# Kernel optimization log

Measured on AMD Instinct MI355X. Metric: run time of the kernel, lower is better.

## Reference

```python
import jax, jax.numpy as jnp
import numpy as np

NEG_INF = -4294967295.0  # -2**32 + 1, matches original padding value

def prelu(x, alpha):
    return jnp.where(x >= 0, x, alpha * x)

def setup_inputs() -> dict:
    key = jax.random.key(0)
    ks = jax.random.split(key, 12)
    B, T, D = 2048, 200, 64
    H0, H1 = 80, 40
    q = jax.random.normal(ks[0], (B, D), dtype=jnp.float32)
    k = jax.random.normal(ks[1], (B, T, D), dtype=jnp.float32)
    v = jax.random.normal(ks[2], (B, T, D), dtype=jnp.float32)
    mask = jax.random.randint(ks[3], (B, T), 0, 2, dtype=jnp.int32)
    Fin = 4 * D  # concat of q, k, q-k, q*k
    W0 = jax.random.normal(ks[4], (Fin, H0), dtype=jnp.float32) / np.sqrt(Fin)
    b0 = jnp.zeros((H0,), dtype=jnp.float32)
    a0 = jax.random.uniform(ks[5], (H0,), dtype=jnp.float32) * 0.25  # PReLU per-feature alpha
    W1 = jax.random.normal(ks[6], (H0, H1), dtype=jnp.float32) / np.sqrt(H0)
    b1 = jnp.zeros((H1,), dtype=jnp.float32)
    a1 = jax.random.uniform(ks[7], (H1,), dtype=jnp.float32) * 0.25
    Wo = jax.random.normal(ks[8], (H1, 1), dtype=jnp.float32) / np.sqrt(H1)
    bo = jnp.zeros((1,), dtype=jnp.float32)
    return {"q": q, "k": k, "v": v, "W0": W0, "b0": b0, "a0": a0,
            "W1": W1, "b1": b1, "a1": a1, "Wo": Wo, "bo": bo, "mask": mask}

def reference(q, k, v, W0, b0, a0, W1, b1, a1, Wo, bo, mask):
    # q: [B,D] -> broadcast to [B,T,D] (tile+reshape in original)
    qe = jnp.broadcast_to(q[:, None, :], k.shape)
    info = jnp.concatenate([qe, k, qe - k, qe * k], axis=-1)  # [B,T,4D]
    h = prelu(jnp.einsum('btf,fh->bth', info, W0) + b0, a0)    # [B,T,H0]
    h = prelu(jnp.einsum('bth,hg->btg', h, W1) + b1, a1)       # [B,T,H1]
    logits = (jnp.einsum('btg,go->bto', h, Wo) + bo)[..., 0]   # [B,T]
    logits = jnp.where(mask == 0, NEG_INF, logits)
    w = jax.nn.softmax(logits, axis=-1)                        # [B,T]
    out = jnp.einsum('bt,btd->bd', w, v)                       # [B,D]
    return out
```

## Files before the change

### kernel.cpp

```cpp
#include <hip/hip_runtime.h>
#include <math.h>

constexpr int D  = 64;
constexpr int T  = 200;
constexpr int H0 = 80;
constexpr int H1 = 40;
constexpr int BLOCK = 256;
constexpr float NEG_INF_V = -4294967295.0f;

typedef short short8 __attribute__((ext_vector_type(8)));
typedef float f32x4 __attribute__((ext_vector_type(4)));

__device__ inline void split_bf16(float x, unsigned short& hi, unsigned short& lo) {
    union { float f; unsigned u; } a; a.f = x;
    unsigned r = a.u + 0x7FFF + ((a.u >> 16) & 1);
    hi = (unsigned short)(r >> 16);
    union { unsigned u; float f; } h; h.u = (unsigned)hi << 16;
    union { float f; unsigned u; } bvu; bvu.f = x - h.f;
    unsigned r2 = bvu.u + 0x7FFF + ((bvu.u >> 16) & 1);
    lo = (unsigned short)(r2 >> 16);
}

__global__ __launch_bounds__(BLOCK, 2) void attn_fused(
    const float* __restrict__ q, const float* __restrict__ k,
    const float* __restrict__ v, const float* __restrict__ W0,
    const float* __restrict__ b0, const float* __restrict__ a0,
    const float* __restrict__ W1, const float* __restrict__ b1,
    const float* __restrict__ a1, const float* __restrict__ Wo,
    const int* __restrict__ mask, float* __restrict__ out)
{
    __shared__ unsigned short s_wfHi[5120];
    __shared__ unsigned short s_wfLo[5120];
    __shared__ unsigned short s_w1Hi[4608];
    __shared__ unsigned short s_w1Lo[4608];
    __shared__ unsigned short s_h0hi[4][16 * 80];
    __shared__ unsigned short s_h0lo[4][16 * 80];
    __shared__ float s_logits[208];
    __shared__ float s_biasq[H0];
    __shared__ float s_a0[H0];
    __shared__ float s_b1p[48], s_a1p[48], s_Wop[48];
    __shared__ float s_w[BLOCK];
    __shared__ float s_red[8];
    __shared__ float s_part[4][D];

    const int tid  = threadIdx.x;
    const int b    = blockIdx.x;
    const int wv   = tid >> 6;
    const int lane = tid & 63;
    const int l16  = lane & 15;
    const int quad = lane >> 4;
    const float* qb = q + (size_t)b * D;

    const int mval = (tid < T) ? mask[(size_t)b * T + tid] : 0;
    float4 kc[4];
    {
        int row = wv * 16 + l16; if (row > T - 1) row = T - 1;
        const float* kr = k + ((size_t)b * T + row) * D + quad * 8;
        kc[0] = *(const float4*)(kr);
        kc[1] = *(const float4*)(kr + 4);
        kc[2] = *(const float4*)(kr + 32);
        kc[3] = *(const float4*)(kr + 36);
    }

    const float* Wk = W0 + 64 * H0;
    const float* Wd = W0 + 128 * H0;
    const float* Wp = W0 + 192 * H0;
    #pragma unroll 4
    for (int it = 0; it < 20; ++it) {
        const int e  = it * 256 + tid;
        const int kk = e / 80, n = e - kk * 80;
        const float w = Wk[e] - Wd[e] + qb[kk] * Wp[e];
        unsigned short h, l; split_bf16(w, h, l);
        const int off = (((kk >> 5) * 5 + (n >> 4)) << 9)
                      + ((((kk >> 3) & 3) * 16 + (n & 15)) << 3) + (kk & 7);
        s_wfHi[off] = h; s_wfLo[off] = l;
    }
    #pragma unroll 4
    for (int it = 0; it < 18; ++it) {
        const int e  = it * 256 + tid;
        const int k2 = e / 48, n = e - k2 * 48;
        const float w = (k2 < H0 && n < H1) ? W1[k2 * H1 + n] : 0.0f;
        unsigned short h, l; split_bf16(w, h, l);
        const int off = (((k2 >> 5) * 3 + (n >> 4)) << 9)
                      + ((((k2 >> 3) & 3) * 16 + (n & 15)) << 3) + (k2 & 7);
        s_w1Hi[off] = h; s_w1Lo[off] = l;
    }
    if (tid < H0) {
        float acc = b0[tid];
        #pragma unroll 8
        for (int d = 0; d < D; ++d)
            acc = fmaf(qb[d], W0[d * H0 + tid] + W0[(128 + d) * H0 + tid], acc);
        s_biasq[tid] = acc;
        s_a0[tid]    = a0[tid];
    }
    if (tid < 48) {
        s_b1p[tid] = (tid < H1) ? b1[tid] : 0.0f;
        s_a1p[tid] = (tid < H1) ? a1[tid] : 0.0f;
        s_Wop[tid] = (tid < H1) ? Wo[tid] : 0.0f;
    }
    __syncthreads();

    for (int mt = wv; mt < 13; mt += 4) {
        float4 kn[4];
        const bool hasNext = (mt + 4 < 13);
        if (hasNext) {
            int row = (mt + 4) * 16 + l16; if (row > T - 1) row = T - 1;
            const float* kr = k + ((size_t)b * T + row) * D + quad * 8;
            kn[0] = *(const float4*)(kr);
            kn[1] = *(const float4*)(kr + 4);
            kn[2] = *(const float4*)(kr + 32);
            kn[3] = *(const float4*)(kr + 36);
        }
        short8 a1hi[2], a1lo[2];
        #pragma unroll
        for (int ks = 0; ks < 2; ++ks) {
            float xs[8] = {kc[ks*2].x, kc[ks*2].y, kc[ks*2].z, kc[ks*2].w,
                           kc[ks*2+1].x, kc[ks*2+1].y, kc[ks*2+1].z, kc[ks*2+1].w};
            #pragma unroll
            for (int j = 0; j < 8; ++j) {
                unsigned short h, l; split_bf16(xs[j], h, l);
                a1hi[ks][j] = (short)h; a1lo[ks][j] = (short)l;
            }
        }
        #pragma unroll
        for (int nt = 0; nt < 5; ++nt) {
            f32x4 acc = {0.0f, 0.0f, 0.0f, 0.0f};
            #pragma unroll
            for (int ks = 0; ks < 2; ++ks) {
                const int off = (ks * 5 + nt) * 512 + lane * 8;
                short8 bh = *(const short8*)&s_wfHi[off];
                short8 bl = *(const short8*)&s_wfLo[off];
                acc = __builtin_amdgcn_mfma_f32_16x16x32_bf16(a1hi[ks], bh, acc, 0, 0, 0);
                acc = __builtin_amdgcn_mfma_f32_16x16x32_bf16(a1hi[ks], bl, acc, 0, 0, 0);
                acc = __builtin_amdgcn_mfma_f32_16x16x32_bf16(a1lo[ks], bh, acc, 0, 0, 0);
            }
            const int h = nt * 16 + l16;
            const float bq = s_biasq[h], al = s_a0[h];
            #pragma unroll
            for (int reg = 0; reg < 4; ++reg) {
                const float x   = acc[reg] + bq;
                const float h0v = (x >= 0.0f) ? x : al * x;
                unsigned short hh, hl; split_bf16(h0v, hh, hl);
                const int addr = (quad * 4 + reg) * 80 + h;
                s_h0hi[wv][addr] = hh;
                s_h0lo[wv][addr] = hl;
            }
        }
        __asm__ __volatile__("s_waitcnt lgkmcnt(0)" ::: "memory");

        short8 a2hi[3], a2lo[3];
        #pragma unroll
        for (int k2s = 0; k2s < 3; ++k2s) {
            if (k2s < 2 || quad < 2) {
                const int addr = l16 * 80 + k2s * 32 + quad * 8;
                a2hi[k2s] = *(const short8*)&s_h0hi[wv][addr];
                a2lo[k2s] = *(const short8*)&s_h0lo[wv][addr];
            } else {
                short8 z = {0, 0, 0, 0, 0, 0, 0, 0};
                a2hi[k2s] = z; a2lo[k2s] = z;
            }
        }
        float part[4] = {0.0f, 0.0f, 0.0f, 0.0f};
        #pragma unroll
        for (int nt2 = 0; nt2 < 3; ++nt2) {
            f32x4 acc = {0.0f, 0.0f, 0.0f, 0.0f};
            #pragma unroll
            for (int k2s = 0; k2s < 3; ++k2s) {
                const int off = (k2s * 3 + nt2) * 512 + lane * 8;
                short8 bh = *(const short8*)&s_w1Hi[off];
                short8 bl = *(const short8*)&s_w1Lo[off];
                acc = __builtin_amdgcn_mfma_f32_16x16x32_bf16(a2hi[k2s], bh, acc, 0, 0, 0);
                acc = __builtin_amdgcn_mfma_f32_16x16x32_bf16(a2hi[k2s], bl, acc, 0, 0, 0);
                acc = __builtin_amdgcn_mfma_f32_16x16x32_bf16(a2lo[k2s], bh, acc, 0, 0, 0);
            }
            const int g = nt2 * 16 + l16;
            const float bg = s_b1p[g], ag = s_a1p[g], wg = s_Wop[g];
            #pragma unroll
            for (int reg = 0; reg < 4; ++reg) {
                const float x  = acc[reg] + bg;
                const float hv = (x >= 0.0f) ? x : ag * x;
                part[reg] = fmaf(hv, wg, part[reg]);
            }
        }
        #pragma unroll
        for (int off = 1; off < 16; off <<= 1) {
            #pragma unroll
            for (int reg = 0; reg < 4; ++reg)
                part[reg] += __shfl_xor(part[reg], off);
        }
        if (l16 == 0) {
            float4 p = {part[0], part[1], part[2], part[3]};
            *(float4*)&s_logits[mt * 16 + quad * 4] = p;
        }
        if (hasNext) {
            #pragma unroll
            for (int i = 0; i < 4; ++i) kc[i] = kn[i];
        }
    }
    __asm__ __volatile__("s_waitcnt lgkmcnt(0)" ::: "memory");
    __syncthreads();

    float logit = -INFINITY;
    if (tid < T)
        logit = (mval == 0) ? NEG_INF_V : s_logits[tid];

    float m = logit;
    #pragma unroll
    for (int off = 32; off > 0; off >>= 1) m = fmaxf(m, __shfl_xor(m, off));
    if (lane == 0) s_red[wv] = m;
    __syncthreads();
    m = fmaxf(fmaxf(s_red[0], s_red[1]), fmaxf(s_red[2], s_red[3]));
    const float e = expf(logit - m);
    s_w[tid] = e;
    float ssum = e;
    #pragma unroll
    for (int off = 32; off > 0; off >>= 1) ssum += __shfl_xor(ssum, off);
    if (lane == 0) s_red[4 + wv] = ssum;
    __syncthreads();
    const float inv = 1.0f / (s_red[4] + s_red[5] + s_red[6] + s_red[7]);

    const int d = tid & (D - 1);
    const int c = tid >> 6;
    constexpr int TC = T / 4;
    float acc2 = 0.0f;
    const float* vp = v + ((size_t)b * T + c * TC) * D + d;
    #pragma unroll 10
    for (int t = 0; t < TC; ++t)
        acc2 = fmaf(s_w[c * TC + t], vp[t * D], acc2);
    s_part[c][d] = acc2;
    __syncthreads();
    if (tid < D) {
        out[(size_t)b * D + tid] =
            (s_part[0][tid] + s_part[1][tid] + s_part[2][tid] + s_part[3][tid]) * inv;
    }
}

extern "C" void kernel_launch(void* const* d_in, const int* in_sizes, int n_in,
                              void* d_out, int out_size, void* d_ws, size_t ws_size,
                              hipStream_t stream) {
    const float* q  = (const float*)d_in[0];
    const float* k  = (const float*)d_in[1];
    const float* v  = (const float*)d_in[2];
    const float* W0 = (const float*)d_in[3];
    const float* b0 = (const float*)d_in[4];
    const float* a0 = (const float*)d_in[5];
    const float* W1 = (const float*)d_in[6];
    const float* b1 = (const float*)d_in[7];
    const float* a1 = (const float*)d_in[8];
    const float* Wo = (const float*)d_in[9];
    const int*  mask = (const int*)d_in[11];
    float* out = (float*)d_out;

    const int B = in_sizes[0] / D;

    attn_fused<<<dim3(B), dim3(BLOCK), 0, stream>>>(
        q, k, v, W0, b0, a0, W1, b1, a1, Wo, mask, out);
}
```

Baseline: 296.7 us.

## Transpose first MFMA to keep hidden activations in registers via bpermute

The first-layer MFMA now uses the weights as the A operand and K as the B operand, so each lane holds four consecutive hidden features. Those values are packed into bf16 pairs and redistributed across lanes with ds_bpermute to form the second-layer operands. This removes the per-wave shared-memory staging buffer for h0 and its wait. Launch bounds move to three blocks per CU now that LDS use is lower. Conversions use the packed bf16 intrinsics in place of the manual bit rounding. The cost is many bpermute operations and extra register pressure under the tighter occupancy bound.

New measurement: 418.4 us. 1.41x slower.

```diff
diff --git a/kernel.cpp b/kernel.cpp
--- a/kernel.cpp
+++ b/kernel.cpp
@@ -1,4 +1,5 @@
 #include <hip/hip_runtime.h>
+#include <hip/hip_bf16.h>
 #include <math.h>
 
 constexpr int D  = 64;
@@ -10,18 +11,21 @@
 
 typedef short short8 __attribute__((ext_vector_type(8)));
 typedef float f32x4 __attribute__((ext_vector_type(4)));
-
-__device__ inline void split_bf16(float x, unsigned short& hi, unsigned short& lo) {
-    union { float f; unsigned u; } a; a.f = x;
-    unsigned r = a.u + 0x7FFF + ((a.u >> 16) & 1);
-    hi = (unsigned short)(r >> 16);
-    union { unsigned u; float f; } h; h.u = (unsigned)hi << 16;
-    union { float f; unsigned u; } bvu; bvu.f = x - h.f;
-    unsigned r2 = bvu.u + 0x7FFF + ((bvu.u >> 16) & 1);
-    lo = (unsigned short)(r2 >> 16);
-}
-
-__global__ __launch_bounds__(BLOCK, 2) void attn_fused(
+typedef int   int4v __attribute__((ext_vector_type(4)));
+
+union S8 { int4v i; short8 s; };
+
+__device__ inline unsigned short bf16h(float x) {
+    __hip_bfloat16 t = __float2bfloat16(x);
+    union { __hip_bfloat16 v; unsigned short u; } c; c.v = t; return c.u;
+}
+__device__ inline unsigned pk_bf16(float a, float b) {
+    float2 f2; f2.x = a; f2.y = b;
+    __hip_bfloat162 t = __float22bfloat162_rn(f2);
+    union { __hip_bfloat162 v; unsigned u; } c; c.v = t; return c.u;
+}
+
+__global__ __launch_bounds__(BLOCK, 3) void attn_fused(
     const float* __restrict__ q, const float* __restrict__ k,
     const float* __restrict__ v, const float* __restrict__ W0,
     const float* __restrict__ b0, const float* __restrict__ a0,
@@ -33,8 +37,6 @@
     __shared__ unsigned short s_wfLo[5120];
     __shared__ unsigned short s_w1Hi[4608];
     __shared__ unsigned short s_w1Lo[4608];
-    __shared__ unsigned short s_h0hi[4][16 * 80];
-    __shared__ unsigned short s_h0lo[4][16 * 80];
     __shared__ float s_logits[208];
     __shared__ float s_biasq[H0];
     __shared__ float s_a0[H0];
@@ -68,22 +70,24 @@
     #pragma unroll 4
     for (int it = 0; it < 20; ++it) {
         const int e  = it * 256 + tid;
-        const int kk = e / 80, n = e - kk * 80;
+        const int kk = e / 80, h = e - kk * 80;
         const float w = Wk[e] - Wd[e] + qb[kk] * Wp[e];
-        unsigned short h, l; split_bf16(w, h, l);
-        const int off = (((kk >> 5) * 5 + (n >> 4)) << 9)
-                      + ((((kk >> 3) & 3) * 16 + (n & 15)) << 3) + (kk & 7);
-        s_wfHi[off] = h; s_wfLo[off] = l;
+        const unsigned short hb = bf16h(w);
+        const unsigned short lb = bf16h(w - __uint_as_float((unsigned)hb << 16));
+        const int off = (((kk >> 5) * 5 + (h >> 4)) << 9)
+                      + (((((kk >> 3) & 3) << 4) + (h & 15)) << 3) + (kk & 7);
+        s_wfHi[off] = hb; s_wfLo[off] = lb;
     }
     #pragma unroll 4
     for (int it = 0; it < 18; ++it) {
         const int e  = it * 256 + tid;
         const int k2 = e / 48, n = e - k2 * 48;
         const float w = (k2 < H0 && n < H1) ? W1[k2 * H1 + n] : 0.0f;
-        unsigned short h, l; split_bf16(w, h, l);
+        const unsigned short hb = bf16h(w);
+        const unsigned short lb = bf16h(w - __uint_as_float((unsigned)hb << 16));
         const int off = (((k2 >> 5) * 3 + (n >> 4)) << 9)
-                      + ((((k2 >> 3) & 3) * 16 + (n & 15)) << 3) + (k2 & 7);
-        s_w1Hi[off] = h; s_w1Lo[off] = l;
+                      + (((((k2 >> 3) & 3) << 4) + (n & 15)) << 3) + (k2 & 7);
+        s_w1Hi[off] = hb; s_w1Lo[off] = lb;
     }
     if (tid < H0) {
         float acc = b0[tid];
@@ -99,6 +103,9 @@
         s_Wop[tid] = (tid < H1) ? Wo[tid] : 0.0f;
     }
     __syncthreads();
+
+    const int addr0 = (((quad & 1) << 5) + l16) << 2;
+    const int addr1 = addr0 + 64;
 
     for (int mt = wv; mt < 13; mt += 4) {
         float4 kn[4];
@@ -111,54 +118,70 @@
             kn[2] = *(const float4*)(kr + 32);
             kn[3] = *(const float4*)(kr + 36);
         }
-        short8 a1hi[2], a1lo[2];
+        short8 kbhi[2], kblo[2];
         #pragma unroll
         for (int ks = 0; ks < 2; ++ks) {
             float xs[8] = {kc[ks*2].x, kc[ks*2].y, kc[ks*2].z, kc[ks*2].w,
                            kc[ks*2+1].x, kc[ks*2+1].y, kc[ks*2+1].z, kc[ks*2+1].w};
-            #pragma unroll
-            for (int j = 0; j < 8; ++j) {
-                unsigned short h, l; split_bf16(xs[j], h, l);
-                a1hi[ks][j] = (short)h; a1lo[ks][j] = (short)l;
-            }
-        }
-        #pragma unroll
-        for (int nt = 0; nt < 5; ++nt) {
+            int wh[4], wl[4];
+            #pragma unroll
+            for (int p = 0; p < 4; ++p) {
+                const unsigned hwd = pk_bf16(xs[2*p], xs[2*p+1]);
+                const float e0 = xs[2*p]   - __uint_as_float(hwd << 16);
+                const float e1 = xs[2*p+1] - __uint_as_float(hwd & 0xffff0000u);
+                wh[p] = (int)hwd; wl[p] = (int)pk_bf16(e0, e1);
+            }
+            S8 uh; uh.i = (int4v){wh[0], wh[1], wh[2], wh[3]}; kbhi[ks] = uh.s;
+            S8 ul; ul.i = (int4v){wl[0], wl[1], wl[2], wl[3]}; kblo[ks] = ul.s;
+        }
+        unsigned hw[5][2], lw[5][2];
+        #pragma unroll
+        for (int ht = 0; ht < 5; ++ht) {
             f32x4 acc = {0.0f, 0.0f, 0.0f, 0.0f};
             #pragma unroll
             for (int ks = 0; ks < 2; ++ks) {
-                const int off = (ks * 5 + nt) * 512 + lane * 8;
-                short8 bh = *(const short8*)&s_wfHi[off];
-                short8 bl = *(const short8*)&s_wfLo[off];
-                acc = __builtin_amdgcn_mfma_f32_16x16x32_bf16(a1hi[ks], bh, acc, 0, 0, 0);
-                acc = __builtin_amdgcn_mfma_f32_16x16x32_bf16(a1hi[ks], bl, acc, 0, 0, 0);
-                acc = __builtin_amdgcn_mfma_f32_16x16x32_bf16(a1lo[ks], bh, acc, 0, 0, 0);
-            }
-            const int h = nt * 16 + l16;
-            const float bq = s_biasq[h], al = s_a0[h];
+                const int off = (ks * 5 + ht) * 512 + lane * 8;
+                short8 Ah = *(const short8*)&s_wfHi[off];
+                short8 Al = *(const short8*)&s_wfLo[off];
+                acc = __builtin_amdgcn_mfma_f32_16x16x32_bf16(Ah, kbhi[ks], acc, 0, 0, 0);
+                acc = __builtin_amdgcn_mfma_f32_16x16x32_bf16(Ah, kblo[ks], acc, 0, 0, 0);
+                acc = __builtin_amdgcn_mfma_f32_16x16x32_bf16(Al, kbhi[ks], acc, 0, 0, 0);
+            }
+            float hf[4];
             #pragma unroll
             for (int reg = 0; reg < 4; ++reg) {
-                const float x   = acc[reg] + bq;
-                const float h0v = (x >= 0.0f) ? x : al * x;
-                unsigned short hh, hl; split_bf16(h0v, hh, hl);
-                const int addr = (quad * 4 + reg) * 80 + h;
-                s_h0hi[wv][addr] = hh;
-                s_h0lo[wv][addr] = hl;
-            }
-        }
-        __asm__ __volatile__("s_waitcnt lgkmcnt(0)" ::: "memory");
-
+                const int h   = ht * 16 + quad * 4 + reg;
+                const float x = acc[reg] + s_biasq[h];
+                hf[reg] = (x >= 0.0f) ? x : s_a0[h] * x;
+            }
+            #pragma unroll
+            for (int p = 0; p < 2; ++p) {
+                const unsigned hwd = pk_bf16(hf[2*p], hf[2*p+1]);
+                const float e0 = hf[2*p]   - __uint_as_float(hwd << 16);
+                const float e1 = hf[2*p+1] - __uint_as_float(hwd & 0xffff0000u);
+                hw[ht][p] = hwd; lw[ht][p] = pk_bf16(e0, e1);
+            }
+        }
         short8 a2hi[3], a2lo[3];
         #pragma unroll
         for (int k2s = 0; k2s < 3; ++k2s) {
-            if (k2s < 2 || quad < 2) {
-                const int addr = l16 * 80 + k2s * 32 + quad * 8;
-                a2hi[k2s] = *(const short8*)&s_h0hi[wv][addr];
-                a2lo[k2s] = *(const short8*)&s_h0lo[wv][addr];
-            } else {
-                short8 z = {0, 0, 0, 0, 0, 0, 0, 0};
-                a2hi[k2s] = z; a2lo[k2s] = z;
-            }
+            int whi[4], wlo[4];
+            #pragma unroll
+            for (int jw = 0; jw < 4; ++jw) {
+                const int p  = jw & 1;
+                const int ad = (jw >> 1) ? addr1 : addr0;
+                const int he = __builtin_amdgcn_ds_bpermute(ad, (int)hw[2*k2s][p]);
+                const int le = __builtin_amdgcn_ds_bpermute(ad, (int)lw[2*k2s][p]);
+                int ho = 0, lo2 = 0;
+                if (k2s < 2) {
+                    ho  = __builtin_amdgcn_ds_bpermute(ad, (int)hw[2*k2s+1][p]);
+                    lo2 = __builtin_amdgcn_ds_bpermute(ad, (int)lw[2*k2s+1][p]);
+                }
+                whi[jw] = (quad >= 2) ? ho  : he;
+                wlo[jw] = (quad >= 2) ? lo2 : le;
+            }
+            S8 uh; uh.i = (int4v){whi[0], whi[1], whi[2], whi[3]}; a2hi[k2s] = uh.s;
+            S8 ul; ul.i = (int4v){wlo[0], wlo[1], wlo[2], wlo[3]}; a2lo[k2s] = ul.s;
         }
         float part[4] = {0.0f, 0.0f, 0.0f, 0.0f};
         #pragma unroll
@@ -197,7 +220,6 @@
             for (int i = 0; i < 4; ++i) kc[i] = kn[i];
         }
     }
-    __asm__ __volatile__("s_waitcnt lgkmcnt(0)" ::: "memory");
     __syncthreads();
 
     float logit = -INFINITY;
```
